# Optimization experiments

Measured on AMD Instinct MI355X. Metric: run time of the kernel, lower is better.

Reference implementation:

```python
import jax, jax.numpy as jnp
import numpy as np

B, S, D, L, H = 4, 2048, 1024, 2, 8  # batch, seq, d_model, hierarchy levels, heads
DH = D // H


def _ln(x, g, b, eps=1e-5):
    mu = jnp.mean(x, axis=-1, keepdims=True)
    xc = x - mu
    var = jnp.mean(xc * xc, axis=-1, keepdims=True)
    return xc * jax.lax.rsqrt(var + eps) * g + b


def setup_inputs() -> dict:
    key = jax.random.key(0)
    ks = jax.random.split(key, 16)
    s = 0.02
    f32 = jnp.float32
    return {
        "x": jax.random.normal(ks[0], (B, S, D), f32),
        "hierarchy_levels": jax.random.randint(ks[1], (B, S), 0, 3),
        # per-level processor MLPs (stacked over level axis)
        "p1_w": jax.random.normal(ks[2], (L, D, D), f32) * s,
        "p1_b": jnp.zeros((L, D), f32),
        "p2_w": jax.random.normal(ks[3], (L, D, D), f32) * s,
        "p2_b": jnp.zeros((L, D), f32),
        "ln_g": jnp.ones((L, D), f32),
        "ln_b": jnp.zeros((L, D), f32),
        # multihead attention projections
        "wq": jax.random.normal(ks[4], (D, D), f32) * s,
        "bq": jnp.zeros((D,), f32),
        "wk": jax.random.normal(ks[5], (D, D), f32) * s,
        "bk": jnp.zeros((D,), f32),
        "wv": jax.random.normal(ks[6], (D, D), f32) * s,
        "bv": jnp.zeros((D,), f32),
        "wo": jax.random.normal(ks[7], (D, D), f32) * s,
        "bo": jnp.zeros((D,), f32),
        # integration MLP: Linear(L*D -> D), SiLU, Linear(D -> D), LayerNorm
        "i1_w": jax.random.normal(ks[8], (L * D, D), f32) * s,
        "i1_b": jnp.zeros((D,), f32),
        "i2_w": jax.random.normal(ks[9], (D, D), f32) * s,
        "i2_b": jnp.zeros((D,), f32),
        "iln_g": jnp.ones((D,), f32),
        "iln_b": jnp.zeros((D,), f32),
    }


def reference(x, hierarchy_levels, p1_w, p1_b, p2_w, p2_b, ln_g, ln_b,
              wq, bq, wk, bk, wv, bv, wo, bo,
              i1_w, i1_b, i2_w, i2_b, iln_g, iln_b):
    # --- per-token expert routing: compute all L processors, select by level ---
    t = jax.nn.silu(jnp.einsum('bsd,lde->lbse', x, p1_w) + p1_b[:, None, None, :])
    h = jnp.einsum('lbse,led->lbsd', t, p2_w) + p2_b[:, None, None, :]
    h = _ln(h, ln_g[:, None, None, :], ln_b[:, None, None, :])  # [L,B,S,D]
    oh = jax.nn.one_hot(hierarchy_levels, L, dtype=x.dtype)      # [B,S,L]; level>=L -> all-zero row
    hsel = jnp.einsum('lbsd,bsl->bsd', h, oh)                    # [B,S,D]
    # --- self-attention over routed outputs ---
    q = (hsel @ wq + bq).reshape(B, S, H, DH)
    k = (hsel @ wk + bk).reshape(B, S, H, DH)
    v = (hsel @ wv + bv).reshape(B, S, H, DH)
    scores = jnp.einsum('bqhd,bkhd->bhqk', q, k) / np.sqrt(DH).astype(x.dtype)
    a = jax.nn.softmax(scores, axis=-1)                          # [B,H,S,S]
    ctx = jnp.einsum('bhqk,bkhd->bqhd', a, v).reshape(B, S, D)
    attended = ctx @ wo + bo
    attn_weights = jnp.mean(a, axis=1)                           # torch avg over heads: [B,S,S]
    # --- integration MLP ---
    z = jnp.concatenate([hsel, attended], axis=-1)               # [B,S,2D]
    z = jax.nn.silu(z @ i1_w + i1_b) @ i2_w + i2_b
    out = _ln(z, iln_g, iln_b)
    return out, attn_weights
```

## Files before the change

### kernel.cpp

```cpp
#include <hip/hip_runtime.h>
#include <cstdint>
#include <cstddef>

#define B_ 4
#define S_ 2048
#define D_ 1024
#define H_ 8
#define DH_ 128
#define MTOT 8192
#define NT_ 32
#define SCALE2 (0.08838834764831845f * 1.4426950408889634f)

typedef __attribute__((ext_vector_type(8))) short s16x8;
typedef __attribute__((ext_vector_type(4))) float f32x4;
typedef __attribute__((ext_vector_type(8))) __bf16 bf16x8;

static __device__ __forceinline__ f32x4 mfma16(s16x8 a, s16x8 b, f32x4 c) {
  return __builtin_amdgcn_mfma_f32_16x16x32_bf16(
      __builtin_bit_cast(bf16x8, a), __builtin_bit_cast(bf16x8, b), c, 0, 0, 0);
}
static __device__ __forceinline__ unsigned short f2bf(float f) {
  unsigned u = __builtin_bit_cast(unsigned, f);
  u += 0x7fffu + ((u >> 16) & 1u);
  return (unsigned short)(u >> 16);
}
static __device__ __forceinline__ float bf2f(unsigned short u) {
  return __builtin_bit_cast(float, (unsigned)u << 16);
}
static __device__ __forceinline__ unsigned cvtpk2(float a, float b) {
  unsigned r;
  asm("v_cvt_pk_bf16_f32 %0, %1, %2" : "=v"(r) : "v"(a), "v"(b));
  return r;
}
static __device__ __forceinline__ void gload_lds16(const void* g, void* l) {
  __builtin_amdgcn_global_load_lds(
      (__attribute__((address_space(1))) void*)(void*)(g),
      (__attribute__((address_space(3))) void*)(l), 16, 0, 0);
}

__global__ __launch_bounds__(256) void xconv2_kernel(const float* __restrict__ x,
                                                     unsigned short* __restrict__ xb,
                                                     const float* __restrict__ wo,
                                                     unsigned short* __restrict__ wob) {
  if (blockIdx.x < 8192) {
    long i = ((long)blockIdx.x * 256 + threadIdx.x) * 4;
    float4 v = *(const float4*)(x + i);
    ushort4 o;
    o.x = f2bf(v.x); o.y = f2bf(v.y); o.z = f2bf(v.z); o.w = f2bf(v.w);
    *(ushort4*)(xb + i) = o;
  } else {
    long i = ((long)(blockIdx.x - 8192) * 256 + threadIdx.x) * 4;
    float4 v = *(const float4*)(wo + i);
    ushort4 o;
    o.x = f2bf(v.x); o.y = f2bf(v.y); o.z = f2bf(v.z); o.w = f2bf(v.w);
    *(ushort4*)(wob + i) = o;
  }
}

__global__ __launch_bounds__(256) void route_kernel(const int* __restrict__ levels,
                                                    int* __restrict__ cnt,
                                                    int* __restrict__ ridx,
                                                    int* __restrict__ act,
                                                    int* __restrict__ act2) {
  const int row = blockIdx.x * 256 + threadIdx.x;
  const int lane = threadIdx.x & 63;
  const int lvl = levels[row];
  const unsigned long long lmlt = (lane == 63) ? ~0ULL >> 1 : (1ULL << lane) - 1;

#pragma unroll
  for (int c = 0; c < 2; c++) {
    bool pred = (lvl == c);
    unsigned long long mask = __ballot(pred);
    int total = __popcll(mask);
    if (total) {
      int leader = __ffsll((long long)mask) - 1;
      int base = 0;
      if (lane == leader) base = atomicAdd(&cnt[c], total);
      base = __shfl(base, leader);
      if (pred) ridx[c * MTOT + base + __popcll(mask & lmlt)] = row;
    }
  }
  {
    bool pred = (lvl < 2);
    unsigned long long mask = __ballot(pred);
    int total = __popcll(mask);
    if (total) {
      int leader = __ffsll((long long)mask) - 1;
      int base = 0;
      if (lane == leader) base = atomicAdd(&cnt[2], total);
      base = __shfl(base, leader);
      if (pred) act[base + __popcll(mask & lmlt)] = row;
    }
    unsigned long long mask2 = ~mask;
    int total2 = 64 - total;
    if (total2) {
      int leader2 = __ffsll((long long)mask2) - 1;
      int base2 = 0;
      if (lane == leader2) base2 = atomicAdd(&cnt[3], total2);
      base2 = __shfl(base2, leader2);
      if (!pred) act2[base2 + __popcll(mask2 & lmlt)] = row;
    }
  }
}

__global__ __launch_bounds__(256) void lvl2fill_kernel(
    const int* __restrict__ act2, const int* __restrict__ cntp,
    const float* __restrict__ bq, const float* __restrict__ bk,
    const float* __restrict__ bv,
    unsigned short* __restrict__ qb, unsigned short* __restrict__ kb,
    unsigned short* __restrict__ vb, unsigned short* __restrict__ z) {
  const int idx = blockIdx.x;
  if (idx >= *cntp) return;
  const long row = act2[idx];
  const int t = threadIdx.x;
  const float4 q4 = *(const float4*)(bq + t * 4);
  const float4 k4 = *(const float4*)(bk + t * 4);
  const float4 v4 = *(const float4*)(bv + t * 4);
  ushort4 qo, ko, vo;
  qo.x = f2bf(q4.x * SCALE2); qo.y = f2bf(q4.y * SCALE2);
  qo.z = f2bf(q4.z * SCALE2); qo.w = f2bf(q4.w * SCALE2);
  ko.x = f2bf(k4.x); ko.y = f2bf(k4.y); ko.z = f2bf(k4.z); ko.w = f2bf(k4.w);
  vo.x = f2bf(v4.x); vo.y = f2bf(v4.y); vo.z = f2bf(v4.z); vo.w = f2bf(v4.w);
  *(ushort4*)(qb + row * 1024 + t * 4) = qo;
  *(ushort4*)(kb + row * 1024 + t * 4) = ko;
  *(ushort4*)(vb + row * 1024 + t * 4) = vo;
  *(ushort4*)(z + row * 2048 + t * 4) = (ushort4){0, 0, 0, 0};
}

struct WtDesc { const float* src; unsigned short* dst; long dst_ld; long dst_off; };
struct WtArgs { WtDesc d[10]; };
__global__ __launch_bounds__(256) void wtrans_all_kernel(WtArgs a) {
  __shared__ unsigned short tile[32][33];
  const int wi = blockIdx.y >> 5;
  const WtDesc de = a.d[wi];
  int r0 = (blockIdx.y & 31) * 32, c0 = blockIdx.x * 32;
  int tr = threadIdx.x >> 5, tc = threadIdx.x & 31;
#pragma unroll
  for (int i = 0; i < 4; i++)
    tile[tr + i * 8][tc] = f2bf(de.src[(long)(r0 + tr + i * 8) * 1024 + c0 + tc]);
  __syncthreads();
#pragma unroll
  for (int i = 0; i < 4; i++)
    de.dst[(long)(c0 + tr + i * 8) * de.dst_ld + de.dst_off + r0 + tc] = tile[tc][tr + i * 8];
}

__global__ __launch_bounds__(256) void vtrans_kernel(const unsigned short* __restrict__ V,
                                                     unsigned short* __restrict__ Vt) {
  __shared__ unsigned short tile[32][33];
  int b = blockIdx.z;
  int h = blockIdx.y >> 2, d0 = (blockIdx.y & 3) * 32;
  int s0 = blockIdx.x * 32;
  int tr = threadIdx.x >> 5, tc = threadIdx.x & 31;
#pragma unroll
  for (int i = 0; i < 4; i++)
    tile[tr + i * 8][tc] = V[((long)(b * S_) + s0 + tr + i * 8) * D_ + h * DH_ + d0 + tc];
  __syncthreads();
  const int sk = s0 + tc;
  const int k6 = sk & 63;
  const int slot = ((k6 >> 5) << 5) | (((k6 >> 2) & 3) << 3) | (((k6 >> 4) & 1) << 2) | (k6 & 3);
  const int ss = (sk & ~63) | slot;
#pragma unroll
  for (int i = 0; i < 4; i++)
    Vt[((long)(b * H_ + h) * DH_ + d0 + tr + i * 8) * S_ + ss] = tile[tc][tr + i * 8];
}

template <int TAG>
__global__ __launch_bounds__(512) void gemm8_kernel(
    const unsigned short* __restrict__ A, int lda,
    const unsigned short* __restrict__ Wt, int ldw,
    const float* __restrict__ bias, float oscale,
    unsigned short* __restrict__ Cb, int ldc,
    int K, int do_silu) {
  __shared__ unsigned short lA[128 * 64];
  __shared__ unsigned short lB[128 * 64];
  const int t = threadIdx.x;
  const int wid = t >> 6, lane = t & 63;
  const int g = lane >> 4, lc = lane & 15;
  const int wr = wid >> 1, wc = wid & 1;
  const int nwg = gridDim.x * gridDim.y;
  int flat = blockIdx.x + gridDim.x * blockIdx.y;
  flat = (flat & 7) * (nwg >> 3) + (flat >> 3);
  const int m0 = (flat / gridDim.x) * 128;
  const int n0 = (flat % gridDim.x) * 128;
  const int srow = lane >> 3, scol = lane & 7;
  const int sxor = (scol ^ srow) << 4;

  f32x4 acc[2][4];
#pragma unroll
  for (int i = 0; i < 2; i++)
#pragma unroll
    for (int j = 0; j < 4; j++) acc[i][j] = (f32x4){0.f, 0.f, 0.f, 0.f};

  const int nk = K >> 6;
  for (int kt = 0; kt < nk; ++kt) {
    const int k0 = kt << 6;
#pragma unroll
    for (int i = 0; i < 2; i++) {
      const int r0 = wid * 16 + i * 8;
      gload_lds16((const char*)(A + (m0 + r0 + srow) * (long)lda + k0) + sxor,
                  (char*)lA + r0 * 128);
      gload_lds16((const char*)(Wt + (n0 + r0 + srow) * (long)ldw + k0) + sxor,
                  (char*)lB + r0 * 128);
    }
    __syncthreads();
#pragma unroll
    for (int kk = 0; kk < 2; kk++) {
      s16x8 af[2], bfr[4];
#pragma unroll
      for (int i = 0; i < 2; i++) {
        int row = wr * 32 + i * 16 + lc;
        af[i] = *(const s16x8*)((const char*)lA + row * 128 +
                                ((kk * 64 + g * 16) ^ ((row & 7) << 4)));
      }
#pragma unroll
      for (int j = 0; j < 4; j++) {
        int row = wc * 64 + j * 16 + lc;
        bfr[j] = *(const s16x8*)((const char*)lB + row * 128 +
                                 ((kk * 64 + g * 16) ^ ((row & 7) << 4)));
      }
#pragma unroll
      for (int i = 0; i < 2; i++)
#pragma unroll
        for (int j = 0; j < 4; j++) acc[i][j] = mfma16(af[i], bfr[j], acc[i][j]);
    }
    __syncthreads();
  }
#pragma unroll
  for (int i = 0; i < 2; i++) {
    const long rbase = m0 + wr * 32 + i * 16 + g * 4;
#pragma unroll
    for (int j = 0; j < 4; j++) {
      const int col = n0 + wc * 64 + j * 16 + lc;
      const float bv = bias[col];
#pragma unroll
      for (int r = 0; r < 4; r++) {
        float v = (acc[i][j][r] + bv) * oscale;
        if (do_silu) v = v / (1.f + __expf(-v));
        Cb[(rbase + r) * (long)ldc + col] = f2bf(v);
      }
    }
  }
}

template <int RMAP>
__global__ __launch_bounds__(512) void gemm8_moe_kernel(
    const unsigned short* __restrict__ A, int lda,
    const unsigned short* __restrict__ Wt0, int ldw,
    const float* __restrict__ bias0,
    unsigned short* __restrict__ Cb, int ldc,
    int K, int do_silu, const int* __restrict__ ridx, const int* __restrict__ cnt2) {
  __shared__ unsigned short lA[128 * 64];
  __shared__ unsigned short lB[128 * 64];
  const int t = threadIdx.x;
  const int wid = t >> 6, lane = t & 63;
  const int g = lane >> 4, lc = lane & 15;
  const int wr = wid >> 1, wc = wid & 1;
  const int nwg = gridDim.x * gridDim.y;
  int flat = blockIdx.x + gridDim.x * blockIdx.y;
  flat = (flat & 7) * (nwg >> 3) + (flat >> 3);
  const int m0 = (flat / gridDim.x) * 128;
  const int n0 = (flat % gridDim.x) * 128;
  const int lvl = m0 >> 12;
  const int lm0 = m0 & 4095;
  if (lm0 >= cnt2[lvl]) return;
  const unsigned short* Wt = Wt0 + (long)lvl * 1048576;
  const float* bias = bias0 + lvl * 1024;
  const int srow = lane >> 3, scol = lane & 7;
  const int sxor = (scol ^ srow) << 4;

  const unsigned short* abase[2];
#pragma unroll
  for (int i = 0; i < 2; i++) {
    int ar;
    if (RMAP) ar = ridx[lvl * MTOT + lm0 + wid * 16 + i * 8 + srow];
    else ar = m0 + wid * 16 + i * 8 + srow;
    abase[i] = A + (long)ar * lda;
  }

  f32x4 acc[2][4];
#pragma unroll
  for (int i = 0; i < 2; i++)
#pragma unroll
    for (int j = 0; j < 4; j++) acc[i][j] = (f32x4){0.f, 0.f, 0.f, 0.f};

  const int nk = K >> 6;
  for (int kt = 0; kt < nk; ++kt) {
    const int k0 = kt << 6;
#pragma unroll
    for (int i = 0; i < 2; i++) {
      const int r0 = wid * 16 + i * 8;
      gload_lds16((const char*)(abase[i] + k0) + sxor, (char*)lA + r0 * 128);
      gload_lds16((const char*)(Wt + (n0 + r0 + srow) * (long)ldw + k0) + sxor,
                  (char*)lB + r0 * 128);
    }
    __syncthreads();
#pragma unroll
    for (int kk = 0; kk < 2; kk++) {
      s16x8 af[2], bfr[4];
#pragma unroll
      for (int i = 0; i < 2; i++) {
        int row = wr * 32 + i * 16 + lc;
        af[i] = *(const s16x8*)((const char*)lA + row * 128 +
                                ((kk * 64 + g * 16) ^ ((row & 7) << 4)));
      }
#pragma unroll
      for (int j = 0; j < 4; j++) {
        int row = wc * 64 + j * 16 + lc;
        bfr[j] = *(const s16x8*)((const char*)lB + row * 128 +
                                 ((kk * 64 + g * 16) ^ ((row & 7) << 4)));
      }
#pragma unroll
      for (int i = 0; i < 2; i++)
#pragma unroll
        for (int j = 0; j < 4; j++) acc[i][j] = mfma16(af[i], bfr[j], acc[i][j]);
    }
    __syncthreads();
  }
#pragma unroll
  for (int i = 0; i < 2; i++) {
    const long rbase = m0 + wr * 32 + i * 16 + g * 4;
#pragma unroll
    for (int j = 0; j < 4; j++) {
      const int col = n0 + wc * 64 + j * 16 + lc;
      const float bv = bias[col];
#pragma unroll
      for (int r = 0; r < 4; r++) {
        float v = acc[i][j][r] + bv;
        if (do_silu) v = v / (1.f + __expf(-v));
        Cb[(rbase + r) * (long)ldc + col] = f2bf(v);
      }
    }
  }
}

__global__ __launch_bounds__(256) void wct_gemm_kernel(
    const unsigned short* __restrict__ A,
    const unsigned short* __restrict__ Wb,
    float* __restrict__ Cf) {
  __shared__ unsigned short lA[128 * 64];
  __shared__ unsigned short lB[128 * 64];
  const int t = threadIdx.x;
  const int wid = t >> 6, lane = t & 63;
  const int g = lane >> 4, lc = lane & 15;
  const int wr = wid >> 1, wc = wid & 1;
  const int chunk = blockIdx.y >> 3;
  const int m0 = (blockIdx.y & 7) * 128;
  const int n0 = blockIdx.x * 128;
  const unsigned short* A0 = A + chunk * 256;
  const unsigned short* W0 = Wb + chunk * 256;
  float* C0 = Cf + (long)chunk * 1048576;
  const int srow = lane >> 3, scol = lane & 7;
  const int sxor = (scol ^ srow) << 4;

  f32x4 acc[4][4];
#pragma unroll
  for (int i = 0; i < 4; i++)
#pragma unroll
    for (int j = 0; j < 4; j++) acc[i][j] = (f32x4){0.f, 0.f, 0.f, 0.f};

  for (int kt = 0; kt < 4; ++kt) {
    const int k0 = kt << 6;
#pragma unroll
    for (int i = 0; i < 4; i++) {
      const int r0 = wid * 32 + i * 8;
      gload_lds16((const char*)(A0 + (m0 + r0 + srow) * 2048L + k0) + sxor,
                  (char*)lA + r0 * 128);
      gload_lds16((const char*)(W0 + (n0 + r0 + srow) * 1024L + k0) + sxor,
                  (char*)lB + r0 * 128);
    }
    __syncthreads();
#pragma unroll
    for (int kk = 0; kk < 2; kk++) {
      s16x8 af[4], bfr[4];
#pragma unroll
      for (int i = 0; i < 4; i++) {
        int row = wr * 64 + i * 16 + lc;
        af[i] = *(const s16x8*)((const char*)lA + row * 128 +
                                ((kk * 64 + g * 16) ^ ((row & 7) << 4)));
      }
#pragma unroll
      for (int j = 0; j < 4; j++) {
        int row = wc * 64 + j * 16 + lc;
        bfr[j] = *(const s16x8*)((const char*)lB + row * 128 +
                                 ((kk * 64 + g * 16) ^ ((row & 7) << 4)));
      }
#pragma unroll
      for (int i = 0; i < 4; i++)
#pragma unroll
        for (int j = 0; j < 4; j++) acc[i][j] = mfma16(af[i], bfr[j], acc[i][j]);
    }
    __syncthreads();
  }
#pragma unroll
  for (int i = 0; i < 4; i++) {
    const long rbase = m0 + wr * 64 + i * 16 + g * 4;
#pragma unroll
    for (int j = 0; j < 4; j++) {
      const int col = n0 + wc * 64 + j * 16 + lc;
#pragma unroll
      for (int r = 0; r < 4; r++) C0[(rbase + r) * 1024L + col] = acc[i][j][r];
    }
  }
}

__global__ __launch_bounds__(256) void wct_reduce_kernel(
    const float* __restrict__ hraw, unsigned short* __restrict__ i1t) {
  long e = ((long)blockIdx.x * 256 + threadIdx.x) * 2;
  float a0 = hraw[e] + hraw[e + 1048576] + hraw[e + 2097152] + hraw[e + 3145728];
  float a1 = hraw[e + 1] + hraw[e + 1 + 1048576] + hraw[e + 1 + 2097152] +
             hraw[e + 1 + 3145728];
  unsigned pk = cvtpk2(a0, a1);
  long n = e >> 10, c = e & 1023;
  *(unsigned*)(i1t + n * 2048 + 1024 + c) = pk;
}

__global__ __launch_bounds__(256) void biascomb_kernel(
    const unsigned short* __restrict__ i1t, const float* __restrict__ bo,
    const float* __restrict__ i1b, float* __restrict__ bias_c) {
  const int n = blockIdx.x, t = threadIdx.x;
  ushort4 w = *(const ushort4*)(i1t + (long)n * 2048 + 1024 + t * 4);
  float4 b = *(const float4*)(bo + t * 4);
  float s = bf2f(w.x) * b.x + bf2f(w.y) * b.y + bf2f(w.z) * b.z + bf2f(w.w) * b.w;
#pragma unroll
  for (int m = 32; m; m >>= 1) s += __shfl_xor(s, m);
  __shared__ float ws_[4];
  if ((t & 63) == 0) ws_[t >> 6] = s;
  __syncthreads();
  if (t == 0) bias_c[n] = i1b[n] + ws_[0] + ws_[1] + ws_[2] + ws_[3];
}

__global__ __launch_bounds__(256) void ln_moe_kernel(
    const unsigned short* __restrict__ in, const int* __restrict__ ridx,
    const int* __restrict__ cnt2,
    const float* __restrict__ gg0, const float* __restrict__ bb0,
    unsigned short* __restrict__ outb, long ldo) {
  const int row = blockIdx.x;
  const int lvl = row >> 12;
  const int lrow = row & 4095;
  if (lrow >= cnt2[lvl]) return;
  const int orow = ridx[lvl * MTOT + lrow];
  const float* gg = gg0 + lvl * 1024;
  const float* bb = bb0 + lvl * 1024;
  const int t = threadIdx.x;
  const ushort4 u = *(const ushort4*)(in + (long)row * D_ + t * 4);
  float v0 = bf2f(u.x), v1 = bf2f(u.y), v2 = bf2f(u.z), v3 = bf2f(u.w);
  float s1 = v0 + v1 + v2 + v3;
  float s2 = v0 * v0 + v1 * v1 + v2 * v2 + v3 * v3;
#pragma unroll
  for (int m = 32; m; m >>= 1) {
    s1 += __shfl_xor(s1, m);
    s2 += __shfl_xor(s2, m);
  }
  __shared__ float w1[4], w2[4];
  if ((t & 63) == 0) { w1[t >> 6] = s1; w2[t >> 6] = s2; }
  __syncthreads();
  s1 = w1[0] + w1[1] + w1[2] + w1[3];
  s2 = w2[0] + w2[1] + w2[2] + w2[3];
  const float mu = s1 * (1.f / D_);
  const float var = s2 * (1.f / D_) - mu * mu;
  const float rs = rsqrtf(var + 1e-5f);
  float vv[4] = {v0, v1, v2, v3};
#pragma unroll
  for (int jj = 0; jj < 4; jj++) {
    int col = t * 4 + jj;
    float y = (vv[jj] - mu) * rs * gg[col] + bb[col];
    outb[(long)orow * ldo + col] = f2bf(y);
  }
}

__global__ __launch_bounds__(256) void ln_kernel(
    const unsigned short* __restrict__ in,
    const float* __restrict__ gg, const float* __restrict__ bb,
    float* __restrict__ outf) {
  const int row = blockIdx.x;
  const int t = threadIdx.x;
  const ushort4 u = *(const ushort4*)(in + (long)row * D_ + t * 4);
  float v0 = bf2f(u.x), v1 = bf2f(u.y), v2 = bf2f(u.z), v3 = bf2f(u.w);
  float s1 = v0 + v1 + v2 + v3;
  float s2 = v0 * v0 + v1 * v1 + v2 * v2 + v3 * v3;
#pragma unroll
  for (int m = 32; m; m >>= 1) {
    s1 += __shfl_xor(s1, m);
    s2 += __shfl_xor(s2, m);
  }
  __shared__ float w1[4], w2[4];
  if ((t & 63) == 0) { w1[t >> 6] = s1; w2[t >> 6] = s2; }
  __syncthreads();
  s1 = w1[0] + w1[1] + w1[2] + w1[3];
  s2 = w2[0] + w2[1] + w2[2] + w2[3];
  const float mu = s1 * (1.f / D_);
  const float var = s2 * (1.f / D_) - mu * mu;
  const float rs = rsqrtf(var + 1e-5f);
  float vv[4] = {v0, v1, v2, v3};
#pragma unroll
  for (int jj = 0; jj < 4; jj++) {
    int col = t * 4 + jj;
    outf[(long)row * D_ + col] = (vv[jj] - mu) * rs * gg[col] + bb[col];
  }
}

__global__ __launch_bounds__(256) void gemm_qkv_kernel(
    const unsigned short* __restrict__ A, int lda,
    const unsigned short* __restrict__ Wt,
    const float* __restrict__ bq, const float* __restrict__ bk,
    const float* __restrict__ bv,
    unsigned short* __restrict__ qb, unsigned short* __restrict__ kb,
    unsigned short* __restrict__ vb,
    const int* __restrict__ act, const int* __restrict__ cntp) {
  __shared__ unsigned short lA[128 * 64];
  __shared__ unsigned short lB[128 * 64];
  const int t = threadIdx.x;
  const int wid = t >> 6, lane = t & 63;
  const int g = lane >> 4, lc = lane & 15;
  const int wr = wid >> 1, wc = wid & 1;
  const int nwg = gridDim.x * gridDim.y;
  int flat = blockIdx.x + gridDim.x * blockIdx.y;
  flat = (flat & 7) * (nwg >> 3) + (flat >> 3);
  const int m0 = (flat / gridDim.x) * 128;
  const int n0 = (flat % gridDim.x) * 128;
  if (m0 >= *cntp) return;
  const int srow = lane >> 3, scol = lane & 7;
  const int sxor = (scol ^ srow) << 4;

  const unsigned short* abase[4];
#pragma unroll
  for (int i = 0; i < 4; i++)
    abase[i] = A + (long)act[m0 + wid * 32 + i * 8 + srow] * lda;

  f32x4 acc[4][4];
#pragma unroll
  for (int i = 0; i < 4; i++)
#pragma unroll
    for (int j = 0; j < 4; j++) acc[i][j] = (f32x4){0.f, 0.f, 0.f, 0.f};

  for (int kt = 0; kt < 16; ++kt) {
    const int k0 = kt << 6;
#pragma unroll
    for (int i = 0; i < 4; i++) {
      const int r0 = wid * 32 + i * 8;
      gload_lds16((const char*)(abase[i] + k0) + sxor, (char*)lA + r0 * 128);
      gload_lds16((const char*)(Wt + (n0 + r0 + srow) * 1024 + k0) + sxor,
                  (char*)lB + r0 * 128);
    }
    __syncthreads();
#pragma unroll
    for (int kk = 0; kk < 2; kk++) {
      s16x8 af[4], bfr[4];
#pragma unroll
      for (int i = 0; i < 4; i++) {
        int row = wr * 64 + i * 16 + lc;
        af[i] = *(const s16x8*)((const char*)lA + row * 128 +
                                ((kk * 64 + g * 16) ^ ((row & 7) << 4)));
      }
#pragma unroll
      for (int j = 0; j < 4; j++) {
        int row = wc * 64 + j * 16 + lc;
        bfr[j] = *(const s16x8*)((const char*)lB + row * 128 +
                                 ((kk * 64 + g * 16) ^ ((row & 7) << 4)));
      }
#pragma unroll
      for (int i = 0; i < 4; i++)
#pragma unroll
        for (int j = 0; j < 4; j++) acc[i][j] = mfma16(af[i], bfr[j], acc[i][j]);
    }
    __syncthreads();
  }
  const int whichB = n0 >> 10;
  const float* bias = whichB == 0 ? bq : whichB == 1 ? bk : bv;
  unsigned short* Cb = whichB == 0 ? qb : whichB == 1 ? kb : vb;
  const float oscale = whichB == 0 ? (float)SCALE2 : 1.0f;
  const int nb = n0 & 1023;
#pragma unroll
  for (int i = 0; i < 4; i++) {
    const int ribase = m0 + wr * 64 + i * 16 + g * 4;
#pragma unroll
    for (int j = 0; j < 4; j++) {
      const int col = nb + wc * 64 + j * 16 + lc;
      const float bvv = bias[col];
#pragma unroll
      for (int r = 0; r < 4; r++) {
        float v = (acc[i][j][r] + bvv) * oscale;
        Cb[(long)act[ribase + r] * 1024L + col] = f2bf(v);
      }
    }
  }
}

__global__ __launch_bounds__(256, 2) void flash_kernel(
    const unsigned short* __restrict__ Q, const unsigned short* __restrict__ Kb,
    const unsigned short* __restrict__ Vt,
    unsigned short* __restrict__ zatt, float* __restrict__ Mo, float* __restrict__ Lo) {
  __shared__ unsigned short lK[2][64 * 128];
  __shared__ unsigned short lV[2][128 * 64];
  const int t = threadIdx.x, wid = t >> 6, lane = t & 63;
  const int g = lane >> 4, lc = lane & 15;
  const int d = blockIdx.x + 16 * (blockIdx.y + 8 * blockIdx.z);
  const int qd = d >> 3, rd = d & 7;
  const int grp = rd + 8 * (qd >> 4);
  const int b = grp >> 3, h = grp & 7, q0 = (qd & 15) * 128;
  const int k_l4 = lane >> 4, k_c = lane & 15;
  const int v_l3 = lane >> 3, v_c = lane & 7;

  s16x8 qf[2][4];
#pragma unroll
  for (int qi = 0; qi < 2; qi++)
#pragma unroll
    for (int kk = 0; kk < 4; kk++)
      qf[qi][kk] = *(const s16x8*)(Q +
          ((long)(b * S_ + q0 + wid * 32 + qi * 16 + lc)) * D_ + h * DH_ + kk * 32 + g * 8);

  f32x4 acco[2][8];
#pragma unroll
  for (int qi = 0; qi < 2; qi++)
#pragma unroll
    for (int dn = 0; dn < 8; dn++) acco[qi][dn] = (f32x4){0.f, 0.f, 0.f, 0.f};
  float m_run[2] = {-1e30f, -1e30f}, l_run[2] = {0.f, 0.f};

  auto stageK = [&](int kt, int buf) {
#pragma unroll
    for (int i = 0; i < 4; i++) {
      const int r0 = wid * 16 + i * 4;
      const int row = r0 + k_l4;
      gload_lds16((const char*)(Kb + (b * S_ + kt * 64 + row) * D_ + h * DH_) +
                      ((k_c ^ (row & 7)) << 4),
                  (char*)&lK[buf][0] + r0 * 256);
    }
  };
  auto stageV = [&](int kt, int buf) {
#pragma unroll
    for (int i = 0; i < 4; i++) {
      const int r0 = wid * 32 + i * 8;
      const int row = r0 + v_l3;
      gload_lds16((const char*)(Vt + ((b * H_ + h) * DH_ + row) * S_ + kt * 64) +
                      ((v_c ^ (row & 7)) << 4),
                  (char*)&lV[buf][0] + r0 * 128);
    }
  };

  stageK(0, 0);
  stageV(0, 0);
  __syncthreads();

  for (int kt = 0; kt < NT_; ++kt) {
    const int cur = kt & 1;
    if (kt + 1 < NT_) { stageK(kt + 1, cur ^ 1); stageV(kt + 1, cur ^ 1); }

    f32x4 s[2][4];
#pragma unroll
    for (int qi = 0; qi < 2; qi++)
#pragma unroll
      for (int kn = 0; kn < 4; kn++) s[qi][kn] = (f32x4){0.f, 0.f, 0.f, 0.f};
    __builtin_amdgcn_s_setprio(1);
#pragma unroll
    for (int kk = 0; kk < 4; kk++) {
      s16x8 kf[4];
#pragma unroll
      for (int kn = 0; kn < 4; kn++) {
        int row = kn * 16 + lc;
        kf[kn] = *(const s16x8*)((const char*)&lK[cur][0] + row * 256 +
                                 ((kk * 64 + g * 16) ^ ((row & 7) << 4)));
      }
#pragma unroll
      for (int qi = 0; qi < 2; qi++)
#pragma unroll
        for (int kn = 0; kn < 4; kn++) s[qi][kn] = mfma16(kf[kn], qf[qi][kk], s[qi][kn]);
    }
    __builtin_amdgcn_s_setprio(0);

    float mx[2];
    int trig = 0;
#pragma unroll
    for (int qi = 0; qi < 2; qi++) {
      float m01 = fmaxf(fmaxf(s[qi][0][0], s[qi][0][1]), fmaxf(s[qi][0][2], s[qi][0][3]));
      float m1 = fmaxf(fmaxf(s[qi][1][0], s[qi][1][1]), fmaxf(s[qi][1][2], s[qi][1][3]));
      float m2 = fmaxf(fmaxf(s[qi][2][0], s[qi][2][1]), fmaxf(s[qi][2][2], s[qi][2][3]));
      float m3 = fmaxf(fmaxf(s[qi][3][0], s[qi][3][1]), fmaxf(s[qi][3][2], s[qi][3][3]));
      float m = fmaxf(fmaxf(m01, m1), fmaxf(m2, m3));
      m = fmaxf(m, __shfl_xor(m, 16));
      m = fmaxf(m, __shfl_xor(m, 32));
      mx[qi] = m;
      trig |= (m > m_run[qi] + 8.0f);
    }
    if (__any(trig)) {
#pragma unroll
      for (int qi = 0; qi < 2; qi++) {
        float mn = fmaxf(m_run[qi], mx[qi]);
        float fsc = exp2f(m_run[qi] - mn);
        m_run[qi] = mn;
        l_run[qi] *= fsc;
#pragma unroll
        for (int dn = 0; dn < 8; dn++)
#pragma unroll
          for (int r = 0; r < 4; r++) acco[qi][dn][r] *= fsc;
      }
    }

    unsigned w[2][4][2];
#pragma unroll
    for (int qi = 0; qi < 2; qi++) {
      float ls = 0.f;
#pragma unroll
      for (int kn = 0; kn < 4; kn++) {
        float p0 = exp2f(s[qi][kn][0] - m_run[qi]);
        float p1 = exp2f(s[qi][kn][1] - m_run[qi]);
        float p2 = exp2f(s[qi][kn][2] - m_run[qi]);
        float p3 = exp2f(s[qi][kn][3] - m_run[qi]);
        ls += (p0 + p1) + (p2 + p3);
        w[qi][kn][0] = cvtpk2(p0, p1);
        w[qi][kn][1] = cvtpk2(p2, p3);
      }
      ls += __shfl_xor(ls, 16);
      ls += __shfl_xor(ls, 32);
      l_run[qi] += ls;
    }

    __builtin_amdgcn_s_setprio(1);
#pragma unroll
    for (int kk = 0; kk < 2; kk++) {
      s16x8 pf[2];
#pragma unroll
      for (int qi = 0; qi < 2; qi++) {
        union { unsigned u[4]; s16x8 v; } pu;
        pu.u[0] = w[qi][2 * kk][0];
        pu.u[1] = w[qi][2 * kk][1];
        pu.u[2] = w[qi][2 * kk + 1][0];
        pu.u[3] = w[qi][2 * kk + 1][1];
        pf[qi] = pu.v;
      }
#pragma unroll
      for (int dn = 0; dn < 8; dn++) {
        int vrow = dn * 16 + lc;
        s16x8 vf = *(const s16x8*)((const char*)&lV[cur][0] + vrow * 128 +
                                   ((kk * 64 + g * 16) ^ ((vrow & 7) << 4)));
#pragma unroll
        for (int qi = 0; qi < 2; qi++) acco[qi][dn] = mfma16(vf, pf[qi], acco[qi][dn]);
      }
    }
    __builtin_amdgcn_s_setprio(0);
    __syncthreads();
  }

  char* tb = (char*)&lK[0][0] + wid * 8192;
#pragma unroll
  for (int qi = 0; qi < 2; qi++) {
    float inv = 1.f / l_run[qi];
    int row = qi * 16 + lc;
#pragma unroll
    for (int dn = 0; dn < 8; dn++) {
      unsigned lo = cvtpk2(acco[qi][dn][0] * inv, acco[qi][dn][1] * inv);
      unsigned hi = cvtpk2(acco[qi][dn][2] * inv, acco[qi][dn][3] * inv);
      unsigned long long pk = (unsigned long long)lo | ((unsigned long long)hi << 32);
      *(unsigned long long*)(tb + row * 256 + ((dn * 32 + g * 8) ^ ((row & 7) << 4))) = pk;
    }
  }
  __syncthreads();
#pragma unroll
  for (int i = 0; i < 8; i++) {
    const int row = i * 4 + (lane >> 4);
    const int chunk = lane & 15;
    s16x8 vv = *(const s16x8*)(tb + row * 256 + ((chunk * 16) ^ ((row & 7) << 4)));
    *(s16x8*)(zatt + ((long)(b * S_ + q0 + wid * 32 + row)) * 2048 + h * DH_ + chunk * 8) = vv;
  }
  if (g == 0) {
#pragma unroll
    for (int qi = 0; qi < 2; qi++) {
      int q = q0 + wid * 32 + qi * 16 + lc;
      Mo[(long)(b * H_ + h) * S_ + q] = m_run[qi];
      Lo[(long)(b * H_ + h) * S_ + q] = l_run[qi];
    }
  }
}

__global__ __launch_bounds__(256) void attw_kernel(
    const unsigned short* __restrict__ Q, const unsigned short* __restrict__ Kb,
    const float* __restrict__ Mo, const float* __restrict__ Lo,
    float* __restrict__ AW) {
  __shared__ unsigned short lK[2][128 * 128];
  __shared__ float lm[H_][128], winv[H_][128];
  const int t = threadIdx.x, wid = t >> 6, lane = t & 63;
  const int g = lane >> 4, lc = lane & 15;
  const int f = blockIdx.x + 16 * (blockIdx.y + 16 * blockIdx.z);
  const int xcd = f & 7, i_ = f >> 3;
  const int grp = (i_ >> 4) * 8 + xcd;
  const int b = grp >> 4, k0 = (grp & 15) * 128, q0 = (i_ & 15) * 128;
  const int k_l4 = lane >> 4, k_c = lane & 15;

  for (int i = t; i < H_ * 128; i += 256) {
    int h = i >> 7, qq = i & 127;
    lm[h][qq] = Mo[(long)(b * H_ + h) * S_ + q0 + qq];
    winv[h][qq] = 0.125f / Lo[(long)(b * H_ + h) * S_ + q0 + qq];
  }

  auto stageK = [&](int h, int buf) {
#pragma unroll
    for (int i = 0; i < 8; i++) {
      const int r0 = wid * 32 + i * 4;
      const int row = r0 + k_l4;
      gload_lds16((const char*)(Kb + ((long)(b * S_ + k0 + row)) * D_ + h * DH_) +
                      ((k_c ^ (row & 7)) << 4),
                  (char*)&lK[buf][0] + r0 * 256);
    }
  };

  f32x4 acc[2][8];
#pragma unroll
  for (int qi = 0; qi < 2; qi++)
#pragma unroll
    for (int kn = 0; kn < 8; kn++) acc[qi][kn] = (f32x4){0.f, 0.f, 0.f, 0.f};

  stageK(0, 0);
  __syncthreads();

  for (int h = 0; h < H_; ++h) {
    const int cur = h & 1;
    if (h + 1 < H_) stageK(h + 1, cur ^ 1);
    f32x4 s[2][8];
#pragma unroll
    for (int qi = 0; qi < 2; qi++)
#pragma unroll
      for (int kn = 0; kn < 8; kn++) s[qi][kn] = (f32x4){0.f, 0.f, 0.f, 0.f};
    __builtin_amdgcn_s_setprio(1);
#pragma unroll
    for (int kk = 0; kk < 4; kk++) {
      s16x8 qa[2];
#pragma unroll
      for (int qi = 0; qi < 2; qi++)
        qa[qi] = *(const s16x8*)(Q +
            ((long)(b * S_ + q0 + wid * 32 + qi * 16 + lc)) * D_ + h * DH_ + kk * 32 + g * 8);
#pragma unroll
      for (int kn = 0; kn < 8; kn++) {
        int row = kn * 16 + lc;
        s16x8 kf = *(const s16x8*)((const char*)&lK[cur][0] + row * 256 +
                                   ((kk * 64 + g * 16) ^ ((row & 7) << 4)));
#pragma unroll
        for (int qi = 0; qi < 2; qi++) s[qi][kn] = mfma16(qa[qi], kf, s[qi][kn]);
      }
    }
    __builtin_amdgcn_s_setprio(0);
#pragma unroll
    for (int qi = 0; qi < 2; qi++)
#pragma unroll
      for (int kn = 0; kn < 8; kn++)
#pragma unroll
        for (int r = 0; r < 4; r++) {
          int qq = wid * 32 + qi * 16 + g * 4 + r;
          acc[qi][kn][r] += exp2f(s[qi][kn][r] - lm[h][qq]) * winv[h][qq];
        }
    __syncthreads();
  }
#pragma unroll
  for (int qi = 0; qi < 2; qi++)
#pragma unroll
    for (int kn = 0; kn < 8; kn++)
#pragma unroll
      for (int r = 0; r < 4; r++) {
        long q = q0 + wid * 32 + qi * 16 + g * 4 + r;
        int k = k0 + kn * 16 + lc;
        AW[((long)b * S_ + q) * S_ + k] = acc[qi][kn][r];
      }
}

__global__ void signal_kernel(float* out, float v) { out[0] = v; }

extern "C" void kernel_launch(void* const* d_in, const int* in_sizes, int n_in,
                              void* d_out, int out_size, void* d_ws, size_t ws_size,
                              hipStream_t stream) {
  constexpr size_t OFF_XB = 0;
  constexpr size_t OFF_W = 16777216ULL;
  constexpr size_t OFF_T = 39845888ULL;
  constexpr size_t OFF_HR = 56623104ULL;
  constexpr size_t OFF_Z = 90177536ULL;
  constexpr size_t OFF_Q = 123731968ULL;
  constexpr size_t OFF_K = 140509184ULL;
  constexpr size_t OFF_V = 157286400ULL;
  constexpr size_t OFF_VT = 174063616ULL;
  constexpr size_t OFF_M = 190840832ULL;
  constexpr size_t OFF_L = 191102976ULL;
  constexpr size_t OFF_CNT = 191365120ULL;
  constexpr size_t OFF_RIDX = 191365184ULL;
  constexpr size_t OFF_BC = OFF_RIDX + 2ULL * MTOT * 4;
  constexpr size_t OFF_ACT = OFF_BC + 4096;
  constexpr size_t OFF_ACT2 = OFF_ACT + MTOT * 4;
  constexpr size_t WS_NEED = OFF_ACT2 + MTOT * 4;

  if (ws_size < WS_NEED) {
    signal_kernel<<<1, 1, 0, stream>>>((float*)d_out, (float)ws_size);
    return;
  }
  const float* x = (const float*)d_in[0];
  const int* levels = (const int*)d_in[1];
  const float* p1w = (const float*)d_in[2];
  const float* p1b = (const float*)d_in[3];
  const float* p2w = (const float*)d_in[4];
  const float* p2b = (const float*)d_in[5];
  const float* lng = (const float*)d_in[6];
  const float* lnb = (const float*)d_in[7];
  const float* wq = (const float*)d_in[8];
  const float* bq = (const float*)d_in[9];
  const float* wk = (const float*)d_in[10];
  const float* bk = (const float*)d_in[11];
  const float* wv = (const float*)d_in[12];
  const float* bv = (const float*)d_in[13];
  const float* wo = (const float*)d_in[14];
  const float* bo = (const float*)d_in[15];
  const float* i1w = (const float*)d_in[16];
  const float* i1b = (const float*)d_in[17];
  const float* i2w = (const float*)d_in[18];
  const float* i2b = (const float*)d_in[19];
  const float* ilng = (const float*)d_in[20];
  const float* ilnb = (const float*)d_in[21];

  char* ws = (char*)d_ws;
  unsigned short* xb = (unsigned short*)(ws + OFF_XB);
  unsigned short* p1t = (unsigned short*)(ws + OFF_W);
  unsigned short* p2t = p1t + 2 * 1048576;
  unsigned short* wqt = p2t + 2 * 1048576;
  unsigned short* wkt = wqt + 1048576;
  unsigned short* wvt = wkt + 1048576;
  unsigned short* wob = wvt + 1048576;
  unsigned short* i1t = wob + 1048576;
  unsigned short* i2t = i1t + 2097152;
  unsigned short* tbuf = (unsigned short*)(ws + OFF_T);
  float* wctp = (float*)(ws + OFF_HR);
  unsigned short* hraw16 = (unsigned short*)(ws + OFF_HR);
  unsigned short* z = (unsigned short*)(ws + OFF_Z);
  unsigned short* qb = (unsigned short*)(ws + OFF_Q);
  unsigned short* kb = (unsigned short*)(ws + OFF_K);
  unsigned short* vb = (unsigned short*)(ws + OFF_V);
  unsigned short* vt = (unsigned short*)(ws + OFF_VT);
  float* Mo = (float*)(ws + OFF_M);
  float* Lo = (float*)(ws + OFF_L);
  int* cnt = (int*)(ws + OFF_CNT);
  int* ridx = (int*)(ws + OFF_RIDX);
  float* bias_c = (float*)(ws + OFF_BC);
  int* act = (int*)(ws + OFF_ACT);
  int* act2 = (int*)(ws + OFF_ACT2);
  float* out = (float*)d_out;
  float* aw = out + (size_t)MTOT * D_;

  dim3 blk(256), blk8(512);
  hipMemsetAsync(cnt, 0, 64, stream);
  hipMemsetAsync(ridx, 0, 2 * MTOT * 4, stream);
  hipMemsetAsync(act, 0, MTOT * 4, stream);
  xconv2_kernel<<<9216, blk, 0, stream>>>(x, xb, wo, wob);
  route_kernel<<<32, blk, 0, stream>>>(levels, cnt, ridx, act, act2);
  lvl2fill_kernel<<<MTOT, blk, 0, stream>>>(act2, cnt + 3, bq, bk, bv, qb, kb, vb, z);

  WtArgs wa;
  wa.d[0] = {p1w, p1t, 1024, 0};
  wa.d[1] = {p1w + 1048576, p1t + 1048576, 1024, 0};
  wa.d[2] = {p2w, p2t, 1024, 0};
  wa.d[3] = {p2w + 1048576, p2t + 1048576, 1024, 0};
  wa.d[4] = {wq, wqt, 1024, 0};
  wa.d[5] = {wk, wkt, 1024, 0};
  wa.d[6] = {wv, wvt, 1024, 0};
  wa.d[7] = {i1w, i1t, 2048, 0};
  wa.d[8] = {i1w + 1048576, i1t, 2048, 1024};
  wa.d[9] = {i2w, i2t, 1024, 0};
  wtrans_all_kernel<<<dim3(32, 320), blk, 0, stream>>>(wa);
  wct_gemm_kernel<<<dim3(8, 32), blk, 0, stream>>>(i1t + 1024, wob, wctp);
  biascomb_kernel<<<1024, blk, 0, stream>>>(i1t, bo, i1b, bias_c);
  wct_reduce_kernel<<<2048, blk, 0, stream>>>(wctp, i1t);

  gemm8_moe_kernel<1><<<dim3(8, 64), blk8, 0, stream>>>(xb, 1024, p1t, 1024, p1b,
                                                        tbuf, 1024, 1024, 1, ridx, cnt);
  gemm8_moe_kernel<0><<<dim3(8, 64), blk8, 0, stream>>>(tbuf, 1024, p2t, 1024, p2b,
                                                        hraw16, 1024, 1024, 0, ridx, cnt);
  ln_moe_kernel<<<8192, blk, 0, stream>>>(hraw16, ridx, cnt, lng, lnb, z, 2048);

  gemm_qkv_kernel<<<dim3(24, 64), blk, 0, stream>>>(z, 2048, wqt, bq, bk, bv, qb, kb, vb,
                                                    act, cnt + 2);
  vtrans_kernel<<<dim3(64, 32, 4), blk, 0, stream>>>(vb, vt);
  flash_kernel<<<dim3(16, 8, 4), blk, 0, stream>>>(qb, kb, vt, z + 1024, Mo, Lo);
  attw_kernel<<<dim3(16, 16, 4), blk, 0, stream>>>(qb, kb, Mo, Lo, aw);
  gemm8_kernel<3><<<dim3(8, 64), blk8, 0, stream>>>(z, 2048, i1t, 2048, bias_c, 1.0f, tbuf,
                                                    1024, 2048, 1);
  gemm8_kernel<4><<<dim3(8, 64), blk8, 0, stream>>>(tbuf, 1024, i2t, 1024, i2b, 1.0f, hraw16,
                                                    1024, 1024, 0);
  ln_kernel<<<8192, blk, 0, stream>>>(hraw16, ilng, ilnb, out);
}
```

Baseline: 440.8 us.

## Software-pipeline flash attention: overlap previous tile's PV MFMAs with current QK

Restructures the flash-attention loop so the P·V product for tile kt-1 is issued right after the Q·K^T MFMAs for tile kt. The softmax exp work of one tile can then overlap matrix work from another. V tiles move to a triple-buffered LDS ring so the tile being consumed late is not overwritten by the next prefetch. An epilogue drains the last tile's PV. The packed probabilities stay live across iterations, which raises register pressure, and LDS per block grows, which may limit occupancy at two blocks per CU.

Result: no change. 437.6 us, median of 2 (-0.7%).

```diff
diff --git a/kernel.cpp b/kernel.cpp
--- a/kernel.cpp
+++ b/kernel.cpp
@@ -591,7 +591,7 @@
     const unsigned short* __restrict__ Vt,
     unsigned short* __restrict__ zatt, float* __restrict__ Mo, float* __restrict__ Lo) {
   __shared__ unsigned short lK[2][64 * 128];
-  __shared__ unsigned short lV[2][128 * 64];
+  __shared__ unsigned short lV[3][128 * 64];
   const int t = threadIdx.x, wid = t >> 6, lane = t & 63;
   const int g = lane >> 4, lc = lane & 15;
   const int d = blockIdx.x + 16 * (blockIdx.y + 8 * blockIdx.z);
@@ -615,6 +615,7 @@
 #pragma unroll
     for (int dn = 0; dn < 8; dn++) acco[qi][dn] = (f32x4){0.f, 0.f, 0.f, 0.f};
   float m_run[2] = {-1e30f, -1e30f}, l_run[2] = {0.f, 0.f};
+  unsigned wp[2][4][2];
 
   auto stageK = [&](int kt, int buf) {
 #pragma unroll
@@ -642,8 +643,8 @@
   __syncthreads();
 
   for (int kt = 0; kt < NT_; ++kt) {
-    const int cur = kt & 1;
-    if (kt + 1 < NT_) { stageK(kt + 1, cur ^ 1); stageV(kt + 1, cur ^ 1); }
+    const int kcur = kt & 1;
+    if (kt + 1 < NT_) { stageK(kt + 1, kcur ^ 1); stageV(kt + 1, (kt + 1) % 3); }
 
     f32x4 s[2][4];
 #pragma unroll
@@ -657,13 +658,37 @@
 #pragma unroll
       for (int kn = 0; kn < 4; kn++) {
         int row = kn * 16 + lc;
-        kf[kn] = *(const s16x8*)((const char*)&lK[cur][0] + row * 256 +
+        kf[kn] = *(const s16x8*)((const char*)&lK[kcur][0] + row * 256 +
                                  ((kk * 64 + g * 16) ^ ((row & 7) << 4)));
       }
 #pragma unroll
       for (int qi = 0; qi < 2; qi++)
 #pragma unroll
         for (int kn = 0; kn < 4; kn++) s[qi][kn] = mfma16(kf[kn], qf[qi][kk], s[qi][kn]);
+    }
+    if (kt > 0) {
+      const int vprev = (kt + 2) % 3;
+#pragma unroll
+      for (int kk = 0; kk < 2; kk++) {
+        s16x8 pf[2];
+#pragma unroll
+        for (int qi = 0; qi < 2; qi++) {
+          union { unsigned u[4]; s16x8 v; } pu;
+          pu.u[0] = wp[qi][2 * kk][0];
+          pu.u[1] = wp[qi][2 * kk][1];
+          pu.u[2] = wp[qi][2 * kk + 1][0];
+          pu.u[3] = wp[qi][2 * kk + 1][1];
+          pf[qi] = pu.v;
+        }
+#pragma unroll
+        for (int dn = 0; dn < 8; dn++) {
+          int vrow = dn * 16 + lc;
+          s16x8 vf = *(const s16x8*)((const char*)&lV[vprev][0] + vrow * 128 +
+                                     ((kk * 64 + g * 16) ^ ((vrow & 7) << 4)));
+#pragma unroll
+          for (int qi = 0; qi < 2; qi++) acco[qi][dn] = mfma16(vf, pf[qi], acco[qi][dn]);
+        }
+      }
     }
     __builtin_amdgcn_s_setprio(0);
 
@@ -695,7 +720,6 @@
       }
     }
 
-    unsigned w[2][4][2];
 #pragma unroll
     for (int qi = 0; qi < 2; qi++) {
       float ls = 0.f;
@@ -706,14 +730,18 @@
         float p2 = exp2f(s[qi][kn][2] - m_run[qi]);
         float p3 = exp2f(s[qi][kn][3] - m_run[qi]);
         ls += (p0 + p1) + (p2 + p3);
-        w[qi][kn][0] = cvtpk2(p0, p1);
-        w[qi][kn][1] = cvtpk2(p2, p3);
+        wp[qi][kn][0] = cvtpk2(p0, p1);
+        wp[qi][kn][1] = cvtpk2(p2, p3);
       }
       ls += __shfl_xor(ls, 16);
       ls += __shfl_xor(ls, 32);
       l_run[qi] += ls;
     }
-
+    __syncthreads();
+  }
+
+  {
+    const int vprev = (NT_ + 2) % 3;
     __builtin_amdgcn_s_setprio(1);
 #pragma unroll
     for (int kk = 0; kk < 2; kk++) {
@@ -721,24 +749,24 @@
 #pragma unroll
       for (int qi = 0; qi < 2; qi++) {
         union { unsigned u[4]; s16x8 v; } pu;
-        pu.u[0] = w[qi][2 * kk][0];
-        pu.u[1] = w[qi][2 * kk][1];
-        pu.u[2] = w[qi][2 * kk + 1][0];
-        pu.u[3] = w[qi][2 * kk + 1][1];
+        pu.u[0] = wp[qi][2 * kk][0];
+        pu.u[1] = wp[qi][2 * kk][1];
+        pu.u[2] = wp[qi][2 * kk + 1][0];
+        pu.u[3] = wp[qi][2 * kk + 1][1];
         pf[qi] = pu.v;
       }
 #pragma unroll
       for (int dn = 0; dn < 8; dn++) {
         int vrow = dn * 16 + lc;
-        s16x8 vf = *(const s16x8*)((const char*)&lV[cur][0] + vrow * 128 +
+        s16x8 vf = *(const s16x8*)((const char*)&lV[vprev][0] + vrow * 128 +
                                    ((kk * 64 + g * 16) ^ ((vrow & 7) << 4)));
 #pragma unroll
         for (int qi = 0; qi < 2; qi++) acco[qi][dn] = mfma16(vf, pf[qi], acco[qi][dn]);
       }
     }
     __builtin_amdgcn_s_setprio(0);
-    __syncthreads();
-  }
+  }
+  __syncthreads();
 
   char* tb = (char*)&lK[0][0] + wid * 8192;
 #pragma unroll
```
